# Kernel optimization log

Measured on AMD Instinct MI355X. Metric: run time of the kernel, lower is better.

## Reference

```python
import jax, jax.numpy as jnp
import numpy as np

N, K, C = 32768, 64, 256
PAIR, HID, BINS, CLIP = 32, 64, 16, 32
LN_EPS = 1e-5


def setup_inputs() -> dict:
    key = jax.random.key(0)
    ks = jax.random.split(key, 12)
    inp = {
        "features": jax.random.normal(ks[0], (N, C), jnp.float32),
        "resi": jnp.arange(N, dtype=jnp.int32),
        "chain": jax.random.randint(ks[1], (N,), 0, 4, jnp.int32),
        "batch": jax.random.randint(ks[2], (N,), 0, 8, jnp.int32),
        "neighbours": jax.random.randint(ks[3], (N, K), 0, N, jnp.int32),
        # learned params
        "W_left": jax.random.normal(ks[4], (C, PAIR), jnp.float32) / np.sqrt(C),
        "W_right": jax.random.normal(ks[5], (C, PAIR), jnp.float32) / np.sqrt(C),
        "W_pos": jax.random.normal(ks[6], (2 * CLIP + 1, PAIR), jnp.float32) * 0.1,
        "ln_scale": jnp.ones((PAIR,), jnp.float32),
        "ln_bias": jnp.zeros((PAIR,), jnp.float32),
        "W1": jax.random.normal(ks[7], (PAIR, HID), jnp.float32) / np.sqrt(PAIR),
        "b1": jnp.zeros((HID,), jnp.float32),
        "W2": jax.random.normal(ks[8], (HID, BINS), jnp.float32) / np.sqrt(HID),
        "b2": jnp.zeros((BINS,), jnp.float32),
    }
    return inp


def reference(features, resi, chain, batch, neighbours,
              W_left, W_right, W_pos, ln_scale, ln_bias, W1, b1, W2, b2):
    # left/right 32-dim codes, pairwise combine via neighbour gather: [N,K,32]
    left = features @ W_left
    right = features @ W_right
    dcode = left[:, None, :] + right[neighbours]

    # relative sequence position one-hot (65 classes) -> Linear(32, bias=False).
    # one_hot @ W_pos == row-gather of W_pos; masked to same chain & batch.
    rel = jnp.clip(resi[neighbours] - resi[:, None], -CLIP, CLIP) + CLIP  # [N,K]
    same = (chain[neighbours] == chain[:, None]) & (batch[neighbours] == batch[:, None])
    dcode = dcode + jnp.where(same[..., None], W_pos[rel], 0.0)

    # LayerNorm over last axis (scale + offset)
    mu = dcode.mean(-1, keepdims=True)
    var = jnp.mean(jnp.square(dcode - mu), -1, keepdims=True)
    dcode = (dcode - mu) * jax.lax.rsqrt(var + LN_EPS) * ln_scale + ln_bias

    # 2-layer GELU MLP -> 16 bins
    h = jax.nn.gelu(dcode @ W1 + b1)
    logits = h @ W2 + b2
    log_p = jax.nn.log_softmax(logits, axis=-1)

    # softmax-weighted expected distance over bin centers of [0, 22) A
    step = 22.0 / BINS
    bin_centers = (jnp.arange(BINS, dtype=jnp.float32) + 0.5) * step
    dmap = (jnp.exp(log_p) * bin_centers).sum(axis=-1)  # [N,K]
    return log_p, dmap
```

## Files before the change

kernel.cpp:

```cpp
#include <hip/hip_runtime.h>
#include <stdint.h>

#define N_RES 32768
#define KNEI  64
#define CFEAT 256
#define PAIRD 32
#define HIDD  64
#define NBINS 16
#define CLIPV 32
#define NGROUPS (N_RES * KNEI / 16)

typedef __attribute__((ext_vector_type(8))) short  short8;
typedef __attribute__((ext_vector_type(4))) float  float4_t;

union U8 { uint32_t u[4]; short8 s8; };

__device__ __forceinline__ uint32_t pkbf(float a, float b) {
    uint32_t ua = __float_as_uint(a) + 0x8000u;
    uint32_t ub = __float_as_uint(b) + 0x8000u;
    uint32_t d;
    const uint32_t sel = 0x07060302u;
    asm("v_perm_b32 %0, %1, %2, %3" : "=v"(d) : "v"(ub), "v"(ua), "s"(sel));
    return d;
}
__device__ __forceinline__ float bflo(uint32_t w) { return __uint_as_float(w << 16); }
__device__ __forceinline__ float bfhi(uint32_t w) { return __uint_as_float(w & 0xFFFF0000u); }

__device__ __forceinline__ float fastrcp(float x) { return __builtin_amdgcn_rcpf(x); }
__device__ __forceinline__ float fexp2(float x)   { return __builtin_amdgcn_exp2f(x); }
__device__ __forceinline__ float flog2(float x)   { return __builtin_amdgcn_logf(x); }

__device__ __forceinline__ float gelu_tanh(float x) {
    const float k1 = 2.3022082f;
    const float k2 = 0.1029432f;
    float x2 = x * x;
    float t  = __builtin_fmaf(k2, x2, k1);
    float e  = fexp2(x * t);
    float th = __builtin_fmaf(-2.0f, fastrcp(e + 1.0f), 1.0f);
    float hx = 0.5f * x;
    return __builtin_fmaf(hx, th, hx);
}

__global__ __launch_bounds__(256) void proj_kernel(
    const float* __restrict__ feat, const float* __restrict__ Wl,
    const float* __restrict__ Wr, const int* __restrict__ resi,
    const int* __restrict__ chain, const int* __restrict__ batch,
    const float* __restrict__ wpos,
    uint4* __restrict__ leftbf, uint4* __restrict__ rightbf,
    uint32_t* __restrict__ meta, uint32_t* __restrict__ wposbf)
{
    __shared__ __align__(16) float Wc[CFEAT * 32];
    const int tid   = threadIdx.x;
    const int half  = blockIdx.x >> 9;
    const int rb    = (blockIdx.x & 511) * 64;
    const float* W  = half ? Wr : Wl;
    uint4* outtb    = half ? rightbf : leftbf;

    for (int idx = tid; idx < CFEAT * 32; idx += 256)
        Wc[idx] = W[idx];
    if (half == 0 && tid < 64) {
        int r = rb + tid;
        meta[r] = (uint32_t)resi[r] | ((uint32_t)chain[r] << 16)
                | ((uint32_t)batch[r] << 19);
    }
    if (blockIdx.x == 0) {
        for (int i = tid; i < (2 * CLIPV + 1) * PAIRD / 2; i += 256)
            wposbf[i] = pkbf(wpos[2 * i], wpos[2 * i + 1]);
    }
    __syncthreads();

    const int cb  = (tid & 3) * 8;
    const int row = rb + (tid >> 2);

    float acc[8];
#pragma unroll
    for (int j = 0; j < 8; ++j) acc[j] = 0.f;

    for (int i = 0; i < CFEAT; i += 4) {
        float4_t f = *(const float4_t*)(feat + (size_t)row * CFEAT + i);
#pragma unroll
        for (int s = 0; s < 4; ++s) {
            float4_t wa = *(const float4_t*)(Wc + (i + s) * 32 + cb);
            float4_t wb = *(const float4_t*)(Wc + (i + s) * 32 + cb + 4);
#pragma unroll
            for (int j = 0; j < 4; ++j) {
                acc[j]     = __builtin_fmaf(f[s], wa[j], acc[j]);
                acc[4 + j] = __builtin_fmaf(f[s], wb[j], acc[4 + j]);
            }
        }
    }
    uint2 o;
    o.x = pkbf(acc[0], acc[1]);
    o.y = pkbf(acc[2], acc[3]);
    uint2 o2;
    o2.x = pkbf(acc[4], acc[5]);
    o2.y = pkbf(acc[6], acc[7]);
    uint2* dst = (uint2*)outtb + (size_t)row * 8 + (cb >> 2);
    dst[0] = o;
    dst[1] = o2;
}

__global__ __launch_bounds__(256, 8) void pair_kernel(
    const uint4* __restrict__ leftbf, const uint4* __restrict__ rightbf,
    const uint32_t* __restrict__ meta, const int* __restrict__ nbr,
    const uint32_t* __restrict__ wposbf,
    const float* __restrict__ lnS, const float* __restrict__ lnB,
    const float* __restrict__ W1, const float* __restrict__ b1,
    const float* __restrict__ W2, const float* __restrict__ b2,
    float* __restrict__ out_logp, float* __restrict__ out_dmap)
{
    __shared__ __align__(16) unsigned char Hbuf[4][16 * 144];
    __shared__ __align__(16) float b1p[HIDD];

    const int tid    = threadIdx.x;
    const int lane   = tid & 63;
    const int wlocal = tid >> 6;
    const int q      = lane >> 4;
    const int c      = lane & 15;

    if (tid < HIDD) {
        float s = b1[tid];
        for (int k = 0; k < PAIRD; ++k)
            s = __builtin_fmaf(lnB[k], W1[k * HIDD + tid], s);
        b1p[tid] = s;
    }

    short8 w1a[4];
#pragma unroll
    for (int t = 0; t < 4; ++t) {
        U8 tmp;
#pragma unroll
        for (int v = 0; v < 4; ++v) {
            int k0 = q * 8 + 2 * v, k1 = k0 + 1;
            float a0 = lnS[k0] * W1[k0 * HIDD + 16 * t + c];
            float a1 = lnS[k1] * W1[k1 * HIDD + 16 * t + c];
            tmp.u[v] = pkbf(a0, a1);
        }
        w1a[t] = tmp.s8;
    }
    short8 w2a[2];
#pragma unroll
    for (int kt = 0; kt < 2; ++kt) {
        U8 tmp;
#pragma unroll
        for (int v = 0; v < 4; ++v) {
            int k0 = kt * 32 + q * 8 + 2 * v;
            tmp.u[v] = pkbf(W2[k0 * NBINS + c], W2[(k0 + 1) * NBINS + c]);
        }
        w2a[kt] = tmp.s8;
    }
    const float4_t b2f = *(const float4_t*)(b2 + 4 * q);

    __syncthreads();

    const int wglobal = (blockIdx.x * 256 + tid) >> 6;
    const int nwaves  = (gridDim.x * 256) >> 6;

    for (int g = wglobal; g < NGROUPS; g += nwaves) {
        const int pbase = g * 16;
        const int n = pbase >> 6;
        const int p = pbase + c;
        const int nb = __builtin_nontemporal_load(nbr + p);

        const uint32_t mn = meta[n];
        const uint32_t mb = meta[nb];
        const uint4 lf = leftbf [(size_t)n  * 4 + q];
        const uint4 rf = rightbf[(size_t)nb * 4 + q];

        const int rel = min(max((int)(mb & 0xFFFFu) - (int)(mn & 0xFFFFu),
                                -CLIPV), CLIPV) + CLIPV;
        const float msk = (((mb ^ mn) & 0xFFFF0000u) == 0u) ? 1.0f : 0.0f;
        const uint4 pw = *(const uint4*)(wposbf + rel * 16 + q * 4);

        const uint32_t la[4] = {lf.x, lf.y, lf.z, lf.w};
        const uint32_t ra[4] = {rf.x, rf.y, rf.z, rf.w};
        const uint32_t pa[4] = {pw.x, pw.y, pw.z, pw.w};
        float d[8];
#pragma unroll
        for (int v = 0; v < 4; ++v) {
            d[2 * v]     = __builtin_fmaf(msk, bflo(pa[v]), bflo(la[v]) + bflo(ra[v]));
            d[2 * v + 1] = __builtin_fmaf(msk, bfhi(pa[v]), bfhi(la[v]) + bfhi(ra[v]));
        }

        float s1 = 0.f, s2 = 0.f;
#pragma unroll
        for (int j = 0; j < 8; ++j) { s1 += d[j]; s2 = __builtin_fmaf(d[j], d[j], s2); }
        s1 += __shfl_xor(s1, 16, 64);  s1 += __shfl_xor(s1, 32, 64);
        s2 += __shfl_xor(s2, 16, 64);  s2 += __shfl_xor(s2, 32, 64);
        const float mu   = s1 * (1.0f / 32.0f);
        const float var  = __builtin_fmaf(-mu, mu, s2 * (1.0f / 32.0f));
        const float rstd = __builtin_amdgcn_rsqf(var + 1e-5f);
        const float sh   = -mu * rstd;

        U8 dpack;
#pragma unroll
        for (int v = 0; v < 4; ++v) {
            float nA = __builtin_fmaf(d[2 * v],     rstd, sh);
            float nB = __builtin_fmaf(d[2 * v + 1], rstd, sh);
            dpack.u[v] = pkbf(nA, nB);
        }
        const short8 dfrag = dpack.s8;

        float4_t hacc[4];
#pragma unroll
        for (int t = 0; t < 4; ++t) {
            float4_t c1 = *(const float4_t*)(b1p + 16 * t + 4 * q);
            hacc[t] = __builtin_amdgcn_mfma_f32_16x16x32_bf16(w1a[t], dfrag, c1, 0, 0, 0);
        }

        unsigned char* hb = &Hbuf[wlocal][0] + c * 144;
#pragma unroll
        for (int t = 0; t < 4; ++t) {
            float g0 = gelu_tanh(hacc[t][0]);
            float g1 = gelu_tanh(hacc[t][1]);
            float g2 = gelu_tanh(hacc[t][2]);
            float g3 = gelu_tanh(hacc[t][3]);
            uint2 w; w.x = pkbf(g0, g1); w.y = pkbf(g2, g3);
            *(uint2*)(hb + 32 * t + 8 * q) = w;
        }
        const short8 hf0 = *(const short8*)(hb + 16 * q);
        const short8 hf1 = *(const short8*)(hb + 64 + 16 * q);

        float4_t lacc;
        lacc = __builtin_amdgcn_mfma_f32_16x16x32_bf16(w2a[0], hf0, b2f,  0, 0, 0);
        lacc = __builtin_amdgcn_mfma_f32_16x16x32_bf16(w2a[1], hf1, lacc, 0, 0, 0);

        const float LOG2E = 1.4426950408889634f, LN2 = 0.6931471805599453f;
        float e[4];
#pragma unroll
        for (int r = 0; r < 4; ++r) e[r] = fexp2(lacc[r] * LOG2E);
        float ssum = (e[0] + e[1]) + (e[2] + e[3]);
        ssum += __shfl_xor(ssum, 16, 64);
        ssum += __shfl_xor(ssum, 32, 64);
        const float lse = flog2(ssum) * LN2;

        float4_t lp = {lacc[0] - lse, lacc[1] - lse, lacc[2] - lse, lacc[3] - lse};
        __builtin_nontemporal_store(lp, (float4_t*)(out_logp + (size_t)p * NBINS + 4 * q));

        const float step  = 22.0f / NBINS;
        const float cbase = (4 * q + 0.5f) * step;
        float dpart = e[0] * cbase + e[1] * (cbase + step)
                    + e[2] * (cbase + 2 * step) + e[3] * (cbase + 3 * step);
        dpart += __shfl_xor(dpart, 16, 64);
        dpart += __shfl_xor(dpart, 32, 64);
        if (q == 0)
            __builtin_nontemporal_store(dpart * fastrcp(ssum), out_dmap + p);
    }
}

extern "C" void kernel_launch(void* const* d_in, const int* in_sizes, int n_in,
                              void* d_out, int out_size, void* d_ws, size_t ws_size,
                              hipStream_t stream) {
    const float* features = (const float*)d_in[0];
    const int*   resi     = (const int*)d_in[1];
    const int*   chain    = (const int*)d_in[2];
    const int*   batch    = (const int*)d_in[3];
    const int*   nbr      = (const int*)d_in[4];
    const float* W_left   = (const float*)d_in[5];
    const float* W_right  = (const float*)d_in[6];
    const float* W_pos    = (const float*)d_in[7];
    const float* ln_scale = (const float*)d_in[8];
    const float* ln_bias  = (const float*)d_in[9];
    const float* W1       = (const float*)d_in[10];
    const float* b1       = (const float*)d_in[11];
    const float* W2       = (const float*)d_in[12];
    const float* b2       = (const float*)d_in[13];

    char* ws = (char*)d_ws;
    uint4*    leftbf  = (uint4*)ws;
    uint4*    rightbf = (uint4*)(ws + (size_t)N_RES * 64);
    uint32_t* meta    = (uint32_t*)(ws + (size_t)2 * N_RES * 64);
    uint32_t* wposbf  = (uint32_t*)(ws + (size_t)2 * N_RES * 64 + N_RES * 4);

    float* out_logp = (float*)d_out;
    float* out_dmap = out_logp + (size_t)N_RES * KNEI * NBINS;

    proj_kernel<<<1024, 256, 0, stream>>>(features, W_left, W_right,
                                          resi, chain, batch, W_pos,
                                          leftbf, rightbf, meta, wposbf);
    pair_kernel<<<2048, 256, 0, stream>>>(leftbf, rightbf, meta, nbr, wposbf,
                                          ln_scale, ln_bias, W1, b1, W2, b2,
                                          out_logp, out_dmap);
}
```

Before: 288.5 us.

## Switch pair pipeline to packed fp16 math with rational GELU approximation

Converts the intermediate storage and MFMA ops from bf16 to fp16. The pair-code assembly, LayerNorm statistics and GELU now run as packed half2 arithmetic, and GELU uses a clamped rational tanh approximation with Newton reciprocal in place of exp2/rcp. The goal is to halve the VALU instruction count in the per-pair elementwise path. In exchange it risks precision loss: LayerNorm sums of squares are accumulated in fp16, and there are overflow/accuracy concerns for large activations.

```diff
diff --git a/kernel.cpp b/kernel.cpp
--- a/kernel.cpp
+++ b/kernel.cpp
@@ -10,35 +10,69 @@
 #define CLIPV 32
 #define NGROUPS (N_RES * KNEI / 16)
 
-typedef __attribute__((ext_vector_type(8))) short  short8;
-typedef __attribute__((ext_vector_type(4))) float  float4_t;
-
-union U8 { uint32_t u[4]; short8 s8; };
-
-__device__ __forceinline__ uint32_t pkbf(float a, float b) {
-    uint32_t ua = __float_as_uint(a) + 0x8000u;
-    uint32_t ub = __float_as_uint(b) + 0x8000u;
-    uint32_t d;
-    const uint32_t sel = 0x07060302u;
-    asm("v_perm_b32 %0, %1, %2, %3" : "=v"(d) : "v"(ub), "v"(ua), "s"(sel));
-    return d;
-}
-__device__ __forceinline__ float bflo(uint32_t w) { return __uint_as_float(w << 16); }
-__device__ __forceinline__ float bfhi(uint32_t w) { return __uint_as_float(w & 0xFFFF0000u); }
+typedef __attribute__((ext_vector_type(2))) _Float16 half2_t;
+typedef __attribute__((ext_vector_type(8))) _Float16 half8_t;
+typedef __attribute__((ext_vector_type(2))) __fp16   fp16v2;
+typedef __attribute__((ext_vector_type(4))) float    float4_t;
+
+union H2U { uint32_t u; half2_t h; fp16v2 f; };
+union V4H { uint4 v; uint32_t u[4]; half2_t h2[4]; };
+union V8H { uint32_t u[4]; half2_t h2[4]; half8_t h8; };
+
+__device__ __forceinline__ uint32_t pkh(float a, float b) {
+    H2U c; c.f = __builtin_amdgcn_cvt_pkrtz(a, b);
+    return c.u;
+}
+__device__ __forceinline__ half2_t pkh2(float a, float b) {
+    H2U c; c.f = __builtin_amdgcn_cvt_pkrtz(a, b);
+    return c.h;
+}
 
 __device__ __forceinline__ float fastrcp(float x) { return __builtin_amdgcn_rcpf(x); }
 __device__ __forceinline__ float fexp2(float x)   { return __builtin_amdgcn_exp2f(x); }
 __device__ __forceinline__ float flog2(float x)   { return __builtin_amdgcn_logf(x); }
 
-__device__ __forceinline__ float gelu_tanh(float x) {
-    const float k1 = 2.3022082f;
-    const float k2 = 0.1029432f;
-    float x2 = x * x;
-    float t  = __builtin_fmaf(k2, x2, k1);
-    float e  = fexp2(x * t);
-    float th = __builtin_fmaf(-2.0f, fastrcp(e + 1.0f), 1.0f);
-    float hx = 0.5f * x;
-    return __builtin_fmaf(hx, th, hx);
+__device__ __forceinline__ uint32_t addph(uint32_t a, uint32_t b) {
+    H2U x, y; x.u = a; y.u = b; x.h = x.h + y.h; return x.u;
+}
+
+__device__ __forceinline__ half2_t gelu2(half2_t x) {
+    const half2_t kA1  = {(_Float16)0.79788456f, (_Float16)0.79788456f};
+    const half2_t kA2  = {(_Float16)0.035677408f,(_Float16)0.035677408f};
+    const half2_t kPA1 = {(_Float16)2.0512820f,  (_Float16)2.0512820f};
+    const half2_t kPA2 = {(_Float16)0.7160840f,  (_Float16)0.7160840f};
+    const half2_t kPA3 = {(_Float16)0.0303104f,  (_Float16)0.0303104f};
+    const half2_t kPB1 = {(_Float16)7.3846154f,  (_Float16)7.3846154f};
+    const half2_t kPB2 = {(_Float16)5.9673660f,  (_Float16)5.9673660f};
+    const half2_t kPB3 = {(_Float16)0.8486920f,  (_Float16)0.8486920f};
+    const half2_t kOne = {(_Float16)1.0f,  (_Float16)1.0f};
+    const half2_t kTwo = {(_Float16)2.0f,  (_Float16)2.0f};
+    const half2_t kQtr = {(_Float16)0.25f, (_Float16)0.25f};
+    const half2_t kHlf = {(_Float16)0.5f,  (_Float16)0.5f};
+    const half2_t kClp = {(_Float16)4.5f,  (_Float16)4.5f};
+    const half2_t kNCl = {(_Float16)-4.5f, (_Float16)-4.5f};
+
+    half2_t u0 = x * x;
+    half2_t y  = x * __builtin_elementwise_fma(kA2, u0, kA1);
+    y = __builtin_elementwise_min(__builtin_elementwise_max(y, kNCl), kClp);
+    half2_t yq = y * kQtr;
+    half2_t v  = yq * yq;
+    half2_t pa = __builtin_elementwise_fma(kPA3, v, kPA2);
+    pa = __builtin_elementwise_fma(pa, v, kPA1);
+    pa = __builtin_elementwise_fma(pa, v, kOne);
+    half2_t pb = __builtin_elementwise_fma(kPB3, v, kPB2);
+    pb = __builtin_elementwise_fma(pb, v, kPB1);
+    pb = __builtin_elementwise_fma(pb, v, kOne);
+    half2_t a = y * pa;
+    H2U cb, cr;
+    cb.h = pb;
+    cr.u = 0x78007800u - cb.u;
+    half2_t r = cr.h;
+    r = r * __builtin_elementwise_fma(-pb, r, kTwo);
+    r = r * __builtin_elementwise_fma(-pb, r, kTwo);
+    half2_t th = a * r;
+    half2_t hx = x * kHlf;
+    return __builtin_elementwise_fma(hx, th, hx);
 }
 
 __global__ __launch_bounds__(256) void proj_kernel(
@@ -65,7 +99,7 @@
     }
     if (blockIdx.x == 0) {
         for (int i = tid; i < (2 * CLIPV + 1) * PAIRD / 2; i += 256)
-            wposbf[i] = pkbf(wpos[2 * i], wpos[2 * i + 1]);
+            wposbf[i] = pkh(wpos[2 * i], wpos[2 * i + 1]);
     }
     __syncthreads();
 
@@ -89,12 +123,11 @@
             }
         }
     }
-    uint2 o;
-    o.x = pkbf(acc[0], acc[1]);
-    o.y = pkbf(acc[2], acc[3]);
-    uint2 o2;
-    o2.x = pkbf(acc[4], acc[5]);
-    o2.y = pkbf(acc[6], acc[7]);
+    uint2 o, o2;
+    o.x  = pkh(acc[0], acc[1]);
+    o.y  = pkh(acc[2], acc[3]);
+    o2.x = pkh(acc[4], acc[5]);
+    o2.y = pkh(acc[6], acc[7]);
     uint2* dst = (uint2*)outtb + (size_t)row * 8 + (cb >> 2);
     dst[0] = o;
     dst[1] = o2;
@@ -125,29 +158,29 @@
         b1p[tid] = s;
     }
 
-    short8 w1a[4];
+    half8_t w1a[4];
 #pragma unroll
     for (int t = 0; t < 4; ++t) {
-        U8 tmp;
+        V8H tmp;
 #pragma unroll
         for (int v = 0; v < 4; ++v) {
             int k0 = q * 8 + 2 * v, k1 = k0 + 1;
             float a0 = lnS[k0] * W1[k0 * HIDD + 16 * t + c];
             float a1 = lnS[k1] * W1[k1 * HIDD + 16 * t + c];
-            tmp.u[v] = pkbf(a0, a1);
-        }
-        w1a[t] = tmp.s8;
-    }
-    short8 w2a[2];
+            tmp.u[v] = pkh(a0, a1);
+        }
+        w1a[t] = tmp.h8;
+    }
+    half8_t w2a[2];
 #pragma unroll
     for (int kt = 0; kt < 2; ++kt) {
-        U8 tmp;
+        V8H tmp;
 #pragma unroll
         for (int v = 0; v < 4; ++v) {
             int k0 = kt * 32 + q * 8 + 2 * v;
-            tmp.u[v] = pkbf(W2[k0 * NBINS + c], W2[(k0 + 1) * NBINS + c]);
-        }
-        w2a[kt] = tmp.s8;
+            tmp.u[v] = pkh(W2[k0 * NBINS + c], W2[(k0 + 1) * NBINS + c]);
+        }
+        w2a[kt] = tmp.h8;
     }
     const float4_t b2f = *(const float4_t*)(b2 + 4 * q);
 
@@ -169,61 +202,66 @@
 
         const int rel = min(max((int)(mb & 0xFFFFu) - (int)(mn & 0xFFFFu),
                                 -CLIPV), CLIPV) + CLIPV;
-        const float msk = (((mb ^ mn) & 0xFFFF0000u) == 0u) ? 1.0f : 0.0f;
+        const uint32_t mskbits = (((mb ^ mn) & 0xFFFF0000u) == 0u)
+                               ? 0x3C003C00u : 0u;
         const uint4 pw = *(const uint4*)(wposbf + rel * 16 + q * 4);
 
-        const uint32_t la[4] = {lf.x, lf.y, lf.z, lf.w};
-        const uint32_t ra[4] = {rf.x, rf.y, rf.z, rf.w};
-        const uint32_t pa[4] = {pw.x, pw.y, pw.z, pw.w};
-        float d[8];
-#pragma unroll
-        for (int v = 0; v < 4; ++v) {
-            d[2 * v]     = __builtin_fmaf(msk, bflo(pa[v]), bflo(la[v]) + bflo(ra[v]));
-            d[2 * v + 1] = __builtin_fmaf(msk, bfhi(pa[v]), bfhi(la[v]) + bfhi(ra[v]));
-        }
-
-        float s1 = 0.f, s2 = 0.f;
-#pragma unroll
-        for (int j = 0; j < 8; ++j) { s1 += d[j]; s2 = __builtin_fmaf(d[j], d[j], s2); }
-        s1 += __shfl_xor(s1, 16, 64);  s1 += __shfl_xor(s1, 32, 64);
-        s2 += __shfl_xor(s2, 16, 64);  s2 += __shfl_xor(s2, 32, 64);
+        V4H lu, ru, pu; lu.v = lf; ru.v = rf; pu.v = pw;
+        H2U mm; mm.u = mskbits;
+        const half2_t m2 = mm.h;
+        half2_t d2[4];
+#pragma unroll
+        for (int v = 0; v < 4; ++v)
+            d2[v] = __builtin_elementwise_fma(pu.h2[v], m2, lu.h2[v] + ru.h2[v]);
+
+        half2_t a1 = (d2[0] + d2[1]) + (d2[2] + d2[3]);
+        half2_t aq = __builtin_elementwise_fma(d2[0], d2[0],
+                     __builtin_elementwise_fma(d2[1], d2[1],
+                     __builtin_elementwise_fma(d2[2], d2[2], d2[3] * d2[3])));
+        H2U c1, c2; c1.h = a1; c2.h = aq;
+        uint32_t s1p = c1.u, s2p = c2.u;
+        s1p = addph(s1p, (uint32_t)__shfl_xor((int)s1p, 16, 64));
+        s1p = addph(s1p, (uint32_t)__shfl_xor((int)s1p, 32, 64));
+        s2p = addph(s2p, (uint32_t)__shfl_xor((int)s2p, 16, 64));
+        s2p = addph(s2p, (uint32_t)__shfl_xor((int)s2p, 32, 64));
+        H2U f1, f2; f1.u = s1p; f2.u = s2p;
+        const float s1 = (float)f1.h[0] + (float)f1.h[1];
+        const float s2 = (float)f2.h[0] + (float)f2.h[1];
         const float mu   = s1 * (1.0f / 32.0f);
         const float var  = __builtin_fmaf(-mu, mu, s2 * (1.0f / 32.0f));
         const float rstd = __builtin_amdgcn_rsqf(var + 1e-5f);
         const float sh   = -mu * rstd;
 
-        U8 dpack;
-#pragma unroll
-        for (int v = 0; v < 4; ++v) {
-            float nA = __builtin_fmaf(d[2 * v],     rstd, sh);
-            float nB = __builtin_fmaf(d[2 * v + 1], rstd, sh);
-            dpack.u[v] = pkbf(nA, nB);
-        }
-        const short8 dfrag = dpack.s8;
+        const half2_t rs2 = pkh2(rstd, rstd);
+        const half2_t sh2 = pkh2(sh, sh);
+        V8H dn;
+#pragma unroll
+        for (int v = 0; v < 4; ++v)
+            dn.h2[v] = __builtin_elementwise_fma(d2[v], rs2, sh2);
+        const half8_t dfrag = dn.h8;
 
         float4_t hacc[4];
 #pragma unroll
         for (int t = 0; t < 4; ++t) {
-            float4_t c1 = *(const float4_t*)(b1p + 16 * t + 4 * q);
-            hacc[t] = __builtin_amdgcn_mfma_f32_16x16x32_bf16(w1a[t], dfrag, c1, 0, 0, 0);
+            float4_t c1v = *(const float4_t*)(b1p + 16 * t + 4 * q);
+            hacc[t] = __builtin_amdgcn_mfma_f32_16x16x32_f16(w1a[t], dfrag, c1v, 0, 0, 0);
         }
 
         unsigned char* hb = &Hbuf[wlocal][0] + c * 144;
 #pragma unroll
         for (int t = 0; t < 4; ++t) {
-            float g0 = gelu_tanh(hacc[t][0]);
-            float g1 = gelu_tanh(hacc[t][1]);
-            float g2 = gelu_tanh(hacc[t][2]);
-            float g3 = gelu_tanh(hacc[t][3]);
-            uint2 w; w.x = pkbf(g0, g1); w.y = pkbf(g2, g3);
-            *(uint2*)(hb + 32 * t + 8 * q) = w;
-        }
-        const short8 hf0 = *(const short8*)(hb + 16 * q);
-        const short8 hf1 = *(const short8*)(hb + 64 + 16 * q);
+            half2_t g01 = gelu2(pkh2(hacc[t][0], hacc[t][1]));
+            half2_t g23 = gelu2(pkh2(hacc[t][2], hacc[t][3]));
+            union { half2_t h[2]; uint2 u2; } w;
+            w.h[0] = g01; w.h[1] = g23;
+            *(uint2*)(hb + 32 * t + 8 * q) = w.u2;
+        }
+        const half8_t hf0 = *(const half8_t*)(hb + 16 * q);
+        const half8_t hf1 = *(const half8_t*)(hb + 64 + 16 * q);
 
         float4_t lacc;
-        lacc = __builtin_amdgcn_mfma_f32_16x16x32_bf16(w2a[0], hf0, b2f,  0, 0, 0);
-        lacc = __builtin_amdgcn_mfma_f32_16x16x32_bf16(w2a[1], hf1, lacc, 0, 0, 0);
+        lacc = __builtin_amdgcn_mfma_f32_16x16x32_f16(w2a[0], hf0, b2f,  0, 0, 0);
+        lacc = __builtin_amdgcn_mfma_f32_16x16x32_f16(w2a[1], hf1, lacc, 0, 0, 0);
 
         const float LOG2E = 1.4426950408889634f, LN2 = 0.6931471805599453f;
         float e[4];
```

New measurement: 327.7 us. +13.6%, slower.
